# Kernel optimization log

Hardware: AMD Instinct MI355X
Metric: run time of the kernel (lower is better)

Reference implementation:

```python
import jax, jax.numpy as jnp
import numpy as np

CONV_LAYERS = 1
BI_GRU_LAYERS = 2
BN_EPS = 1e-3


def _bn(x, gamma, beta, mean, var):
    return gamma * (x - mean) * jax.lax.rsqrt(var + BN_EPS) + beta


def _gru_pass(x, Wx, Wh, b_in, b_rec, reverse=False):
    # Keras GRU: reset_after=True, recurrent_activation=sigmoid, activation=relu,
    # gate order [z, r, h]. x: [B,T,D] -> [B,T,U]
    B, T, _ = x.shape
    U = Wh.shape[0]
    if reverse:
        x = x[:, ::-1]
    xg = jnp.einsum('btd,dg->btg', x, Wx) + b_in  # [B,T,3U] input-side gates, precomputed
    xg = jnp.swapaxes(xg, 0, 1)                    # time-major [T,B,3U]

    def step(h, g):
        rg = h @ Wh + b_rec                        # recurrent-side gates [B,3U]
        xz, xr, xh = jnp.split(g, 3, axis=-1)
        rz, rr, rh = jnp.split(rg, 3, axis=-1)
        z = jax.nn.sigmoid(xz + rz)
        r = jax.nn.sigmoid(xr + rr)
        hh = jax.nn.relu(xh + r * rh)              # reset_after: r gates the recurrent term
        h = z * h + (1.0 - z) * hh
        return h, h

    h0 = jnp.zeros((B, U), x.dtype)
    _, hs = jax.lax.scan(step, h0, xg)             # [T,B,U]
    hs = jnp.swapaxes(hs, 0, 1)
    if reverse:
        hs = hs[:, ::-1]
    return hs


def setup_inputs() -> dict:
    key = jax.random.key(0)
    ks = jax.random.split(key, 16)
    B, T, F = 32, 1024, 80
    C, U, V, K = 512, 512, 1024, 11
    s = 0.02
    inp = {
        'x': jax.random.normal(ks[0], (B, T, F), jnp.float32),
        'conv_w': jax.random.normal(ks[1], (K, F, C), jnp.float32) * s,
        'conv_b': jnp.zeros((C,), jnp.float32),
        'gru_fwd_wx': jax.random.normal(ks[2], (C, 3 * U), jnp.float32) * s,
        'gru_fwd_wh': jax.random.normal(ks[3], (U, 3 * U), jnp.float32) * s,
        'gru_fwd_bi': jnp.zeros((3 * U,), jnp.float32),
        'gru_fwd_br': jnp.zeros((3 * U,), jnp.float32),
        'gru_bwd_wx': jax.random.normal(ks[4], (C, 3 * U), jnp.float32) * s,
        'gru_bwd_wh': jax.random.normal(ks[5], (U, 3 * U), jnp.float32) * s,
        'gru_bwd_bi': jnp.zeros((3 * U,), jnp.float32),
        'gru_bwd_br': jnp.zeros((3 * U,), jnp.float32),
        'gamma': jnp.ones((C,), jnp.float32) + 0.1 * jax.random.normal(ks[6], (C,), jnp.float32),
        'beta': 0.1 * jax.random.normal(ks[7], (C,), jnp.float32),
        'mov_mean': jnp.zeros((C,), jnp.float32),
        'mov_var': jnp.ones((C,), jnp.float32),
        'dense_w': jax.random.normal(ks[8], (U, V), jnp.float32) * s,
        'dense_b': jnp.zeros((V,), jnp.float32),
    }
    return inp


def reference(x, conv_w, conv_b, gru_fwd_wx, gru_fwd_wh, gru_fwd_bi, gru_fwd_br,
              gru_bwd_wx, gru_bwd_wh, gru_bwd_bi, gru_bwd_br,
              gamma, beta, mov_mean, mov_var, dense_w, dense_b):
    for _ in range(CONV_LAYERS):
        x = jax.lax.conv_general_dilated(
            x, conv_w, window_strides=(2,), padding='SAME',
            dimension_numbers=('NWC', 'WIO', 'NWC'))
        x = jax.nn.relu(x + conv_b)
    x = _bn(x, gamma, beta, mov_mean, mov_var)  # same BN layer reused in source
    for _ in range(BI_GRU_LAYERS):              # same BiGRU layer (shared weights) reused
        x = (_gru_pass(x, gru_fwd_wx, gru_fwd_wh, gru_fwd_bi, gru_fwd_br, reverse=False)
             + _gru_pass(x, gru_bwd_wx, gru_bwd_wh, gru_bwd_bi, gru_bwd_br, reverse=True))
    x = _bn(x, gamma, beta, mov_mean, mov_var)
    logits = jnp.einsum('btu,uv->btv', x, dense_w) + dense_b
    return jax.nn.softmax(logits, axis=-1)
```

## Files before the change

kernel.cpp:

```cpp
#include <hip/hip_runtime.h>
#include <hip/hip_fp16.h>

#define BB 32
#define CC 512
#define UU 512
#define GG 1536
#define VV 1024
#define TT 512
#define MM (BB*TT)
#define TIN 1024
#define FIN 80
#define EPS 1e-3f
#define SENT 0xFFFFFFFFu

typedef _Float16 h8 __attribute__((ext_vector_type(8)));
typedef float f4 __attribute__((ext_vector_type(4)));

__global__ __launch_bounds__(256) void conv_bn_k(
    const float* __restrict__ x, const float* __restrict__ w, const float* __restrict__ cb,
    const float* __restrict__ gam, const float* __restrict__ bet,
    const float* __restrict__ mu_, const float* __restrict__ var_,
    __half* __restrict__ out)
{
  __shared__ float xs[41*80];
  int tg = blockIdx.x, b = blockIdx.y, ch = blockIdx.z;
  int t0 = tg*16;
  int in0 = t0*2 - 4;
  for (int i = threadIdx.x; i < 41*80; i += 256) {
    int r = i / 80, f = i - r*80;
    int ri = in0 + r;
    xs[i] = (ri >= 0 && ri < TIN) ? x[((size_t)b*TIN + ri)*FIN + f] : 0.f;
  }
  __syncthreads();
  int c = ch*256 + threadIdx.x;
  float acc[16];
  float bv = cb[c];
#pragma unroll
  for (int i = 0; i < 16; i++) acc[i] = bv;
  for (int k = 0; k < 11; k++) {
    for (int f = 0; f < 80; f++) {
      float wv = w[((size_t)k*80 + f)*CC + c];
#pragma unroll
      for (int i = 0; i < 16; i++) acc[i] += xs[(2*i + k)*80 + f] * wv;
    }
  }
  float ga = gam[c], be = bet[c], mu = mu_[c], iv = rsqrtf(var_[c] + EPS);
#pragma unroll
  for (int i = 0; i < 16; i++) {
    float v = fmaxf(acc[i], 0.f);
    out[((size_t)b*TT + t0 + i)*CC + c] = __float2half(ga*(v - mu)*iv + be);
  }
}

__global__ __launch_bounds__(256) void prep_wx_k(
    const float* __restrict__ wxf, const float* __restrict__ wxb,
    __half* __restrict__ of, __half* __restrict__ ob)
{
  __shared__ float tile[64][65];
  int kt = blockIdx.x*64, nt = blockIdx.y*64;
  const float* src = blockIdx.z ? wxb : wxf;
  __half* dst = blockIdx.z ? ob : of;
  for (int i = threadIdx.x; i < 4096; i += 256) {
    int r = i >> 6, c = i & 63;
    tile[r][c] = src[(size_t)(kt+r)*GG + nt + c];
  }
  __syncthreads();
  for (int i = threadIdx.x; i < 4096; i += 256) {
    int r = i >> 6, c = i & 63;
    __half h = __float2half(tile[c][r]);
    dst[(size_t)(nt+r)*1024 + kt + c] = h;
    dst[(size_t)(nt+r)*1024 + 512 + kt + c] = h;
  }
}

__global__ __launch_bounds__(256) void prep_dense_k(
    const float* __restrict__ dw, const float* __restrict__ gam, const float* __restrict__ var_,
    __half* __restrict__ dst)
{
  __shared__ float tile[64][65];
  __shared__ float s64[64];
  int kt = blockIdx.x*64, nt = blockIdx.y*64;
  if (threadIdx.x < 64) {
    int k = kt + threadIdx.x;
    s64[threadIdx.x] = gam[k] * rsqrtf(var_[k] + EPS);
  }
  for (int i = threadIdx.x; i < 4096; i += 256) {
    int r = i >> 6, c = i & 63;
    tile[r][c] = dw[(size_t)(kt+r)*VV + nt + c];
  }
  __syncthreads();
  for (int i = threadIdx.x; i < 4096; i += 256) {
    int r = i >> 6, c = i & 63;
    __half h = __float2half(tile[c][r] * s64[c]);
    dst[(size_t)(nt+r)*1024 + kt + c] = h;
    dst[(size_t)(nt+r)*1024 + 512 + kt + c] = h;
  }
}

__global__ __launch_bounds__(256) void prep_bias_k(
    const float* __restrict__ dw, const float* __restrict__ db,
    const float* __restrict__ gam, const float* __restrict__ bet,
    const float* __restrict__ mu_, const float* __restrict__ var_,
    float* __restrict__ bias2)
{
  int n = blockIdx.x*256 + threadIdx.x;
  float acc = db[n];
  for (int k = 0; k < CC; k++) {
    float o = bet[k] - gam[k]*mu_[k]*rsqrtf(var_[k] + EPS);
    acc += o * dw[(size_t)k*VV + n];
  }
  bias2[n] = acc;
}

template<int OUTH>
__global__ __launch_bounds__(256,2) void hgemm_k(
    const __half* __restrict__ A, const __half* __restrict__ BT,
    const float* __restrict__ bias, void* __restrict__ Cout,
    int M, int N, int K, int lda, int ldb)
{
  __shared__ _Float16 As[2][128*40];
  __shared__ _Float16 Bs[2][128*40];
  int m0 = blockIdx.y*128, n0 = blockIdx.x*128;
  int tid = threadIdx.x;
  int l = tid & 63, w = tid >> 6;
  int wr = w >> 1, wc = w & 1;
  int srow = tid >> 1, soff = (tid & 1)*16;
  const __half* ap = A  + (size_t)(m0 + srow)*lda + soff;
  const __half* bp = BT + (size_t)(n0 + srow)*ldb + soff;
  f4 acc[4][4];
#pragma unroll
  for (int i=0;i<4;i++)
#pragma unroll
    for (int j=0;j<4;j++) acc[i][j] = (f4){0.f,0.f,0.f,0.f};

  uint4 av  = *(const uint4*)(ap);
  uint4 av2 = *(const uint4*)(ap + 8);
  uint4 bv  = *(const uint4*)(bp);
  uint4 bv2 = *(const uint4*)(bp + 8);
  *(uint4*)&As[0][srow*40 + soff]     = av;
  *(uint4*)&As[0][srow*40 + soff + 8] = av2;
  *(uint4*)&Bs[0][srow*40 + soff]     = bv;
  *(uint4*)&Bs[0][srow*40 + soff + 8] = bv2;
  __syncthreads();

  int lr = (l & 15), lk = (l >> 4)*8;
  int nk = K >> 5;
  for (int kt = 0; kt < nk; kt++) {
    int cb_ = kt & 1;
    if (kt + 1 < nk) {
      av  = *(const uint4*)(ap + kt*32 + 32);
      av2 = *(const uint4*)(ap + kt*32 + 40);
      bv  = *(const uint4*)(bp + kt*32 + 32);
      bv2 = *(const uint4*)(bp + kt*32 + 40);
    }
    h8 af[4], bf[4];
#pragma unroll
    for (int i = 0; i < 4; i++)
      af[i] = *(const h8*)&As[cb_][(wr*64 + i*16 + lr)*40 + lk];
#pragma unroll
    for (int j = 0; j < 4; j++)
      bf[j] = *(const h8*)&Bs[cb_][(wc*64 + j*16 + lr)*40 + lk];
#pragma unroll
    for (int i = 0; i < 4; i++)
#pragma unroll
      for (int j = 0; j < 4; j++)
        acc[i][j] = __builtin_amdgcn_mfma_f32_16x16x32_f16(af[i], bf[j], acc[i][j], 0, 0, 0);
    if (kt + 1 < nk) {
      *(uint4*)&As[cb_^1][srow*40 + soff]     = av;
      *(uint4*)&As[cb_^1][srow*40 + soff + 8] = av2;
      *(uint4*)&Bs[cb_^1][srow*40 + soff]     = bv;
      *(uint4*)&Bs[cb_^1][srow*40 + soff + 8] = bv2;
    }
    __syncthreads();
  }
  int cb = n0 + wc*64 + lr;
  int rb = m0 + wr*64 + (l >> 4)*4;
#pragma unroll
  for (int j = 0; j < 4; j++) {
    float bs = bias[cb + j*16];
#pragma unroll
    for (int i = 0; i < 4; i++) {
#pragma unroll
      for (int q = 0; q < 4; q++) {
        float v = acc[i][j][q] + bs;
        int row = rb + i*16 + q, col = cb + j*16;
        if (OUTH) ((__half*)Cout)[(size_t)row*N + col] = __float2half(v);
        else      ((float*)Cout)[(size_t)row*N + col] = v;
      }
    }
  }
}

__global__ __launch_bounds__(256,1) void gru_layer_k(
    const __half* __restrict__ xgf, const __half* __restrict__ xgb,
    const float* __restrict__ whf, const float* __restrict__ whb,
    const float* __restrict__ brf, const float* __restrict__ brb,
    __half* __restrict__ H,
    unsigned* __restrict__ hbL)
{
  int wg  = blockIdx.x & 7;
  int bg  = (blockIdx.x >> 3) & 3;
  int dir = blockIdx.x >> 5;
  int grp = dir*4 + bg;
  const __half* xg = dir ? xgb : xgf;
  const float* wh  = dir ? whb : whf;
  const float* brc = dir ? brb : brf;
  unsigned* hbg = hbL + (size_t)grp*8192;
  int tid = threadIdx.x;
  int L = tid & 63, wv = tid >> 6;
  int u0 = wg*64, b0 = bg*8;

  __shared__ _Float16 hsl[2][8][544];

  int urow = L & 15, kb = L >> 4;
  int ubase = u0 + wv*16;
  h8 wb[3][16];
#pragma unroll
  for (int g3 = 0; g3 < 3; g3++)
#pragma unroll
    for (int ks = 0; ks < 16; ks++) {
      h8 v;
#pragma unroll
      for (int j = 0; j < 8; j++)
        v[j] = (_Float16)wh[(size_t)(ks*32 + kb*8 + j)*GG + g3*512 + ubase + urow];
      wb[g3][ks] = v;
    }

  int b = L & 15, b7 = L & 7;
  int myu = ubase + kb*4;
  float br3[3][4];
#pragma unroll
  for (int g3 = 0; g3 < 3; g3++)
#pragma unroll
    for (int q = 0; q < 4; q++)
      br3[g3][q] = brc[g3*512 + myu + q];
  float hreg[4] = {0.f, 0.f, 0.f, 0.f};
  bool bval = b < 8;
  int upair = (u0 >> 1) + wv*8 + kb*2;

  uint2 xz2, xr2, xh2;
  {
    int t0_ = dir ? 511 : 0;
    const unsigned* xp = (const unsigned*)xg + (size_t)((b0 + b7)*TT + t0_)*768;
    xz2 = *(const uint2*)(xp + upair);
    xr2 = *(const uint2*)(xp + 256 + upair);
    xh2 = *(const uint2*)(xp + 512 + upair);
  }

  (void)__hip_atomic_exchange(&hbg[0*2048 + wg*256 + tid], 0u,
                              __ATOMIC_RELAXED, __HIP_MEMORY_SCOPE_AGENT);

  int sr = tid >> 5, sc = tid & 31;
  int sb = sc >> 2, sg0 = sr*8 + (sc & 3)*2;
  int sws0 = ((sg0 ^ sb) << 3), sws1 = (((sg0 + 1) ^ sb) << 3);

#define STAGE(PH, NB) {                                                     \
    const unsigned* gp = &hbg[(PH)*2048 + sr*256 + sc*8];                   \
    uint4 d0, d1;                                                           \
    long guard = 0;                                                         \
    for (;;) {                                                              \
      asm volatile(                                                         \
        "global_load_dwordx4 %0, %2, off sc0 sc1\n\t"                       \
        "global_load_dwordx4 %1, %2, off offset:16 sc0 sc1\n\t"             \
        "s_waitcnt vmcnt(0)"                                                \
        : "=&v"(d0), "=&v"(d1) : "v"(gp) : "memory");                       \
      bool ok = (d0.x!=SENT)&(d0.y!=SENT)&(d0.z!=SENT)&(d0.w!=SENT)         \
              & (d1.x!=SENT)&(d1.y!=SENT)&(d1.z!=SENT)&(d1.w!=SENT);        \
      if (ok || ++guard > 2000000L) break;                                  \
      if (guard > 2) __builtin_amdgcn_s_sleep(1);                           \
    }                                                                       \
    *(uint4*)&hsl[NB][sb][sws0] = d0;                                       \
    *(uint4*)&hsl[NB][sb][sws1] = d1;                                       \
  }

  STAGE(0, 0);
  __syncthreads();

  for (int s = 0; s < 512; s++) {
    int buf = s & 1;
    f4 a0 = (f4){0.f,0.f,0.f,0.f}, a1 = a0, a2 = a0;
#pragma unroll
    for (int ks = 0; ks < 16; ks++) {
      int g = ks*4 + kb;
      h8 hf = *(const h8*)&hsl[buf][b7][(g ^ b7) << 3];
      a0 = __builtin_amdgcn_mfma_f32_16x16x32_f16(wb[0][ks], hf, a0, 0, 0, 0);
      a1 = __builtin_amdgcn_mfma_f32_16x16x32_f16(wb[1][ks], hf, a1, 0, 0, 0);
      a2 = __builtin_amdgcn_mfma_f32_16x16x32_f16(wb[2][ks], hf, a2, 0, 0, 0);
    }
    int t = dir ? (511 - s) : s;
    __half2 xzl = *(__half2*)&xz2.x, xzh = *(__half2*)&xz2.y;
    __half2 xrl = *(__half2*)&xr2.x, xrh = *(__half2*)&xr2.y;
    __half2 xhl = *(__half2*)&xh2.x, xhh = *(__half2*)&xh2.y;
    float2 fz0 = __half22float2(xzl), fz1 = __half22float2(xzh);
    float2 fr0 = __half22float2(xrl), fr1 = __half22float2(xrh);
    float2 fh0 = __half22float2(xhl), fh1 = __half22float2(xhh);
    float xzf[4] = {fz0.x, fz0.y, fz1.x, fz1.y};
    float xrf[4] = {fr0.x, fr0.y, fr1.x, fr1.y};
    float xhf[4] = {fh0.x, fh0.y, fh1.x, fh1.y};
#pragma unroll
    for (int q = 0; q < 4; q++) {
      float az = (q==0? a0[0] : q==1? a0[1] : q==2? a0[2] : a0[3]);
      float ar = (q==0? a1[0] : q==1? a1[1] : q==2? a1[2] : a1[3]);
      float ah = (q==0? a2[0] : q==1? a2[1] : q==2? a2[2] : a2[3]);
      float z = 1.f/(1.f + __expf(-(xzf[q] + br3[0][q] + az)));
      float r = 1.f/(1.f + __expf(-(xrf[q] + br3[1][q] + ar)));
      float hh = fmaxf(xhf[q] + r*(br3[2][q] + ah), 0.f);
      hreg[q] = z*hreg[q] + (1.f - z)*hh;
    }
    int pn = (s + 1) & 3;
    if (bval) {
      __half2 p01 = __floats2half2_rn(hreg[0], hreg[1]);
      __half2 p23 = __floats2half2_rn(hreg[2], hreg[3]);
      unsigned pk0 = *(unsigned*)&p01, pk1 = *(unsigned*)&p23;
      unsigned long long pkl = ((unsigned long long)pk1 << 32) | pk0;
      (void)__hip_atomic_exchange(
          (unsigned long long*)&hbg[pn*2048 + wg*256 + b*32 + wv*8 + kb*2],
          pkl, __ATOMIC_RELAXED, __HIP_MEMORY_SCOPE_AGENT);
      uint2 pv; pv.x = pk0; pv.y = pk1;
      *(uint2*)((unsigned*)H + (size_t)((b0 + b)*TT + t)*512 + dir*256 + upair) = pv;
    }
    {
      int tn = (dir ? (510 - s) : (s + 1)) & 511;
      const unsigned* xp = (const unsigned*)xg + (size_t)((b0 + b7)*TT + tn)*768;
      xz2 = *(const uint2*)(xp + upair);
      xr2 = *(const uint2*)(xp + 256 + upair);
      xh2 = *(const uint2*)(xp + 512 + upair);
    }
    if (s < 511) STAGE(pn, buf ^ 1);
    if (tid < 128)
      (void)__hip_atomic_exchange(
          (unsigned long long*)&hbg[((s+3)&3)*2048 + wg*256] + tid,
          0xFFFFFFFFFFFFFFFFull, __ATOMIC_RELAXED, __HIP_MEMORY_SCOPE_AGENT);
    __syncthreads();
  }
#undef STAGE
}

__global__ __launch_bounds__(256) void softmax_k(float* __restrict__ p) {
  size_t row = blockIdx.x;
  float* pr = p + row*VV;
  int tid = threadIdx.x;
  float4 v = ((float4*)pr)[tid];
  float m = fmaxf(fmaxf(v.x, v.y), fmaxf(v.z, v.w));
#pragma unroll
  for (int o = 32; o >= 1; o >>= 1) m = fmaxf(m, __shfl_xor(m, o));
  __shared__ float red[4];
  __shared__ float red2[4];
  int w = tid >> 6;
  if ((tid & 63) == 0) red[w] = m;
  __syncthreads();
  m = fmaxf(fmaxf(red[0], red[1]), fmaxf(red[2], red[3]));
  v.x = __expf(v.x - m); v.y = __expf(v.y - m);
  v.z = __expf(v.z - m); v.w = __expf(v.w - m);
  float s = v.x + v.y + v.z + v.w;
#pragma unroll
  for (int o = 32; o >= 1; o >>= 1) s += __shfl_xor(s, o);
  if ((tid & 63) == 0) red2[w] = s;
  __syncthreads();
  s = red2[0] + red2[1] + red2[2] + red2[3];
  float inv = 1.f / s;
  v.x *= inv; v.y *= inv; v.z *= inv; v.w *= inv;
  ((float4*)pr)[tid] = v;
}

extern "C" void kernel_launch(void* const* d_in, const int* in_sizes, int n_in,
                              void* d_out, int out_size, void* d_ws, size_t ws_size,
                              hipStream_t stream) {
  const float* x      = (const float*)d_in[0];
  const float* conv_w = (const float*)d_in[1];
  const float* conv_b = (const float*)d_in[2];
  const float* wx_f   = (const float*)d_in[3];
  const float* wh_f   = (const float*)d_in[4];
  const float* bi_f   = (const float*)d_in[5];
  const float* br_f   = (const float*)d_in[6];
  const float* wx_b   = (const float*)d_in[7];
  const float* wh_b   = (const float*)d_in[8];
  const float* bi_b   = (const float*)d_in[9];
  const float* br_b   = (const float*)d_in[10];
  const float* gam    = (const float*)d_in[11];
  const float* bet    = (const float*)d_in[12];
  const float* mu_    = (const float*)d_in[13];
  const float* var_   = (const float*)d_in[14];
  const float* dw     = (const float*)d_in[15];
  const float* db     = (const float*)d_in[16];

  char* ws = (char*)d_ws;
  __half* xgf   = (__half*)(ws + 0);
  __half* xgb   = (__half*)(ws + 50331648LL);
  __half* WxfT2 = (__half*)(ws + 100663296LL);
  __half* WxbT2 = (__half*)(ws + 103809024LL);
  __half* DwT2  = (__half*)(ws + 106954752LL);
  float*  bias2 = (float*)(ws + 109051904LL);
  __half* c0    = (__half*)(ws + 109056000LL);
  __half* H     = (__half*)(ws + 109056000LL);
  unsigned* hb1 = (unsigned*)(ws + 142610432LL);
  unsigned* hb2 = (unsigned*)(ws + 142872576LL);
  if (ws_size < 143134720ULL) return;
  float* logits = (float*)d_out;

  (void)hipMemsetAsync(hb1, 0xFF, 524288, stream);

  prep_wx_k<<<dim3(8,24,2), 256, 0, stream>>>(wx_f, wx_b, WxfT2, WxbT2);
  prep_dense_k<<<dim3(8,16), 256, 0, stream>>>(dw, gam, var_, DwT2);
  prep_bias_k<<<4, 256, 0, stream>>>(dw, db, gam, bet, mu_, var_, bias2);

  conv_bn_k<<<dim3(32,32,2), 256, 0, stream>>>(x, conv_w, conv_b, gam, bet, mu_, var_, c0);

  hgemm_k<1><<<dim3(12,128), 256, 0, stream>>>(c0, WxfT2, bi_f, xgf, MM, GG, 512, 512, 1024);
  hgemm_k<1><<<dim3(12,128), 256, 0, stream>>>(c0, WxbT2, bi_b, xgb, MM, GG, 512, 512, 1024);
  gru_layer_k<<<64, 256, 0, stream>>>(xgf, xgb, wh_f, wh_b, br_f, br_b, H, hb1);
  hgemm_k<1><<<dim3(12,128), 256, 0, stream>>>(H, WxfT2, bi_f, xgf, MM, GG, 1024, 1024, 1024);
  hgemm_k<1><<<dim3(12,128), 256, 0, stream>>>(H, WxbT2, bi_b, xgb, MM, GG, 1024, 1024, 1024);
  gru_layer_k<<<64, 256, 0, stream>>>(xgf, xgb, wh_f, wh_b, br_f, br_b, H, hb2);
  hgemm_k<0><<<dim3(8,128), 256, 0, stream>>>(H, DwT2, bias2, logits, MM, VV, 1024, 1024, 1024);
  softmax_k<<<MM, 256, 0, stream>>>(logits);
}
```

Before: 2.832 ms.

## Overlap next-layer projection GEMMs with GRU recurrence via persistent worker blocks

```diff
diff --git a/kernel.cpp b/kernel.cpp
--- a/kernel.cpp
+++ b/kernel.cpp
@@ -191,68 +191,142 @@
   }
 }
 
-__global__ __launch_bounds__(256,1) void gru_layer_k(
+__device__ __forceinline__ void worker_tile(
+    const unsigned short* __restrict__ Hh, const __half* __restrict__ BT,
+    const float* __restrict__ bias, void* __restrict__ Cout,
+    int m0, int n0, int N, int OUTH,
+    _Float16* As, _Float16* Bs, int tid)
+{
+  int l = tid & 63, w = tid >> 6;
+  int wr = w >> 1, wc = w & 1;
+  int srow = tid >> 1, soff = (tid & 1)*16;
+  const __half* bp = BT + (size_t)(n0 + srow)*1024 + soff;
+  const unsigned short* apB = Hh + (size_t)(m0 + srow)*1024 + soff;
+  f4 acc[4][4];
+#pragma unroll
+  for (int i=0;i<4;i++)
+#pragma unroll
+    for (int j=0;j<4;j++) acc[i][j] = (f4){0.f,0.f,0.f,0.f};
+  int lr = (l & 15), lk = (l >> 4)*8;
+  for (int kt = 0; kt < 32; kt++) {
+    uint4 a0, a1;
+    const unsigned short* gpa = apB + kt*32;
+    asm volatile(
+      "global_load_dwordx4 %0, %2, off sc0 sc1\n\t"
+      "global_load_dwordx4 %1, %2, off offset:16 sc0 sc1\n\t"
+      "s_waitcnt vmcnt(0)"
+      : "=&v"(a0), "=&v"(a1) : "v"(gpa) : "memory");
+    uint4 b0 = *(const uint4*)(bp + kt*32);
+    uint4 b1 = *(const uint4*)(bp + kt*32 + 8);
+    __syncthreads();
+    *(uint4*)&As[srow*40 + soff]     = a0;
+    *(uint4*)&As[srow*40 + soff + 8] = a1;
+    *(uint4*)&Bs[srow*40 + soff]     = b0;
+    *(uint4*)&Bs[srow*40 + soff + 8] = b1;
+    __syncthreads();
+    h8 af[4], bf[4];
+#pragma unroll
+    for (int i = 0; i < 4; i++)
+      af[i] = *(const h8*)&As[(wr*64 + i*16 + lr)*40 + lk];
+#pragma unroll
+    for (int j = 0; j < 4; j++)
+      bf[j] = *(const h8*)&Bs[(wc*64 + j*16 + lr)*40 + lk];
+#pragma unroll
+    for (int i = 0; i < 4; i++)
+#pragma unroll
+      for (int j = 0; j < 4; j++)
+        acc[i][j] = __builtin_amdgcn_mfma_f32_16x16x32_f16(af[i], bf[j], acc[i][j], 0, 0, 0);
+  }
+  int cb = n0 + wc*64 + lr;
+  int rb = m0 + wr*64 + (l >> 4)*4;
+#pragma unroll
+  for (int j = 0; j < 4; j++) {
+    float bs = bias[cb + j*16];
+#pragma unroll
+    for (int i = 0; i < 4; i++) {
+#pragma unroll
+      for (int q = 0; q < 4; q++) {
+        float v = acc[i][j][q] + bs;
+        int row = rb + i*16 + q, col = cb + j*16;
+        if (OUTH) ((__half*)Cout)[(size_t)row*N + col] = __float2half(v);
+        else      ((float*)Cout)[(size_t)row*N + col] = v;
+      }
+    }
+  }
+}
+
+template<int L>
+__global__ __launch_bounds__(256,1) void gru_fused_k(
     const __half* __restrict__ xgf, const __half* __restrict__ xgb,
     const float* __restrict__ whf, const float* __restrict__ whb,
     const float* __restrict__ brf, const float* __restrict__ brb,
     __half* __restrict__ H,
-    unsigned* __restrict__ hbL)
-{
-  int wg  = blockIdx.x & 7;
-  int bg  = (blockIdx.x >> 3) & 3;
-  int dir = blockIdx.x >> 5;
-  int grp = dir*4 + bg;
-  const __half* xg = dir ? xgb : xgf;
-  const float* wh  = dir ? whb : whf;
-  const float* brc = dir ? brb : brf;
-  unsigned* hbg = hbL + (size_t)grp*8192;
+    unsigned* __restrict__ hbL,
+    const __half* __restrict__ BTa, const __half* __restrict__ BTb,
+    const float* __restrict__ bsa, const float* __restrict__ bsb,
+    void* __restrict__ outA, void* __restrict__ outB,
+    unsigned* __restrict__ flags, unsigned* __restrict__ queue)
+{
   int tid = threadIdx.x;
-  int L = tid & 63, wv = tid >> 6;
-  int u0 = wg*64, b0 = bg*8;
-
   __shared__ _Float16 hsl[2][8][544];
-
-  int urow = L & 15, kb = L >> 4;
-  int ubase = u0 + wv*16;
-  h8 wb[3][16];
-#pragma unroll
-  for (int g3 = 0; g3 < 3; g3++)
-#pragma unroll
-    for (int ks = 0; ks < 16; ks++) {
-      h8 v;
-#pragma unroll
-      for (int j = 0; j < 8; j++)
-        v[j] = (_Float16)wh[(size_t)(ks*32 + kb*8 + j)*GG + g3*512 + ubase + urow];
-      wb[g3][ks] = v;
-    }
-
-  int b = L & 15, b7 = L & 7;
-  int myu = ubase + kb*4;
-  float br3[3][4];
-#pragma unroll
-  for (int g3 = 0; g3 < 3; g3++)
-#pragma unroll
-    for (int q = 0; q < 4; q++)
-      br3[g3][q] = brc[g3*512 + myu + q];
-  float hreg[4] = {0.f, 0.f, 0.f, 0.f};
-  bool bval = b < 8;
-  int upair = (u0 >> 1) + wv*8 + kb*2;
-
-  uint2 xz2, xr2, xh2;
-  {
-    int t0_ = dir ? 511 : 0;
-    const unsigned* xp = (const unsigned*)xg + (size_t)((b0 + b7)*TT + t0_)*768;
-    xz2 = *(const uint2*)(xp + upair);
-    xr2 = *(const uint2*)(xp + 256 + upair);
-    xh2 = *(const uint2*)(xp + 512 + upair);
-  }
-
-  (void)__hip_atomic_exchange(&hbg[0*2048 + wg*256 + tid], 0u,
-                              __ATOMIC_RELAXED, __HIP_MEMORY_SCOPE_AGENT);
-
-  int sr = tid >> 5, sc = tid & 31;
-  int sb = sc >> 2, sg0 = sr*8 + (sc & 3)*2;
-  int sws0 = ((sg0 ^ sb) << 3), sws1 = (((sg0 + 1) ^ sb) << 3);
+  __shared__ _Float16 As[128*40];
+  __shared__ _Float16 Bs[128*40];
+  __shared__ unsigned tileS;
+
+  if (blockIdx.x < 64) {
+    int wg  = blockIdx.x & 7;
+    int bg  = (blockIdx.x >> 3) & 3;
+    int dir = blockIdx.x >> 5;
+    int grp = dir*4 + bg;
+    const __half* xg = dir ? xgb : xgf;
+    const float* wh  = dir ? whb : whf;
+    const float* brc = dir ? brb : brf;
+    unsigned* hbg = hbL + (size_t)grp*8192;
+    unsigned* myflag = flags + dir*32 + bg*8 + wg;
+    int L_ = tid & 63, wv = tid >> 6;
+    int u0 = wg*64, b0 = bg*8;
+
+    int urow = L_ & 15, kb = L_ >> 4;
+    int ubase = u0 + wv*16;
+    h8 wb[3][16];
+#pragma unroll
+    for (int g3 = 0; g3 < 3; g3++)
+#pragma unroll
+      for (int ks = 0; ks < 16; ks++) {
+        h8 v;
+#pragma unroll
+        for (int j = 0; j < 8; j++)
+          v[j] = (_Float16)wh[(size_t)(ks*32 + kb*8 + j)*GG + g3*512 + ubase + urow];
+        wb[g3][ks] = v;
+      }
+
+    int b = L_ & 15, b7 = L_ & 7;
+    int myu = ubase + kb*4;
+    float br3[3][4];
+#pragma unroll
+    for (int g3 = 0; g3 < 3; g3++)
+#pragma unroll
+      for (int q = 0; q < 4; q++)
+        br3[g3][q] = brc[g3*512 + myu + q];
+    float hreg[4] = {0.f, 0.f, 0.f, 0.f};
+    bool bval = b < 8;
+    int upair = (u0 >> 1) + wv*8 + kb*2;
+
+    uint2 xz2, xr2, xh2;
+    {
+      int t0_ = dir ? 511 : 0;
+      const unsigned* xp = (const unsigned*)xg + (size_t)((b0 + b7)*TT + t0_)*768;
+      xz2 = *(const uint2*)(xp + upair);
+      xr2 = *(const uint2*)(xp + 256 + upair);
+      xh2 = *(const uint2*)(xp + 512 + upair);
+    }
+
+    (void)__hip_atomic_exchange(&hbg[0*2048 + wg*256 + tid], 0u,
+                                __ATOMIC_RELAXED, __HIP_MEMORY_SCOPE_AGENT);
+
+    int sr = tid >> 5, sc = tid & 31;
+    int sb = sc >> 2, sg0 = sr*8 + (sc & 3)*2;
+    int sws0 = ((sg0 ^ sb) << 3), sws1 = (((sg0 + 1) ^ sb) << 3);
 
 #define STAGE(PH, NB) {                                                     \
     const unsigned* gp = &hbg[(PH)*2048 + sr*256 + sc*8];                   \
@@ -273,67 +347,126 @@
     *(uint4*)&hsl[NB][sb][sws1] = d1;                                       \
   }
 
-  STAGE(0, 0);
-  __syncthreads();
-
-  for (int s = 0; s < 512; s++) {
-    int buf = s & 1;
-    f4 a0 = (f4){0.f,0.f,0.f,0.f}, a1 = a0, a2 = a0;
-#pragma unroll
-    for (int ks = 0; ks < 16; ks++) {
-      int g = ks*4 + kb;
-      h8 hf = *(const h8*)&hsl[buf][b7][(g ^ b7) << 3];
-      a0 = __builtin_amdgcn_mfma_f32_16x16x32_f16(wb[0][ks], hf, a0, 0, 0, 0);
-      a1 = __builtin_amdgcn_mfma_f32_16x16x32_f16(wb[1][ks], hf, a1, 0, 0, 0);
-      a2 = __builtin_amdgcn_mfma_f32_16x16x32_f16(wb[2][ks], hf, a2, 0, 0, 0);
-    }
-    int t = dir ? (511 - s) : s;
-    __half2 xzl = *(__half2*)&xz2.x, xzh = *(__half2*)&xz2.y;
-    __half2 xrl = *(__half2*)&xr2.x, xrh = *(__half2*)&xr2.y;
-    __half2 xhl = *(__half2*)&xh2.x, xhh = *(__half2*)&xh2.y;
-    float2 fz0 = __half22float2(xzl), fz1 = __half22float2(xzh);
-    float2 fr0 = __half22float2(xrl), fr1 = __half22float2(xrh);
-    float2 fh0 = __half22float2(xhl), fh1 = __half22float2(xhh);
-    float xzf[4] = {fz0.x, fz0.y, fz1.x, fz1.y};
-    float xrf[4] = {fr0.x, fr0.y, fr1.x, fr1.y};
-    float xhf[4] = {fh0.x, fh0.y, fh1.x, fh1.y};
-#pragma unroll
-    for (int q = 0; q < 4; q++) {
-      float az = (q==0? a0[0] : q==1? a0[1] : q==2? a0[2] : a0[3]);
-      float ar = (q==0? a1[0] : q==1? a1[1] : q==2? a1[2] : a1[3]);
-      float ah = (q==0? a2[0] : q==1? a2[1] : q==2? a2[2] : a2[3]);
-      float z = 1.f/(1.f + __expf(-(xzf[q] + br3[0][q] + az)));
-      float r = 1.f/(1.f + __expf(-(xrf[q] + br3[1][q] + ar)));
-      float hh = fmaxf(xhf[q] + r*(br3[2][q] + ah), 0.f);
-      hreg[q] = z*hreg[q] + (1.f - z)*hh;
-    }
-    int pn = (s + 1) & 3;
-    if (bval) {
-      __half2 p01 = __floats2half2_rn(hreg[0], hreg[1]);
-      __half2 p23 = __floats2half2_rn(hreg[2], hreg[3]);
-      unsigned pk0 = *(unsigned*)&p01, pk1 = *(unsigned*)&p23;
-      unsigned long long pkl = ((unsigned long long)pk1 << 32) | pk0;
-      (void)__hip_atomic_exchange(
-          (unsigned long long*)&hbg[pn*2048 + wg*256 + b*32 + wv*8 + kb*2],
-          pkl, __ATOMIC_RELAXED, __HIP_MEMORY_SCOPE_AGENT);
-      uint2 pv; pv.x = pk0; pv.y = pk1;
-      *(uint2*)((unsigned*)H + (size_t)((b0 + b)*TT + t)*512 + dir*256 + upair) = pv;
-    }
-    {
-      int tn = (dir ? (510 - s) : (s + 1)) & 511;
-      const unsigned* xp = (const unsigned*)xg + (size_t)((b0 + b7)*TT + tn)*768;
-      xz2 = *(const uint2*)(xp + upair);
-      xr2 = *(const uint2*)(xp + 256 + upair);
-      xh2 = *(const uint2*)(xp + 512 + upair);
-    }
-    if (s < 511) STAGE(pn, buf ^ 1);
-    if (tid < 128)
-      (void)__hip_atomic_exchange(
-          (unsigned long long*)&hbg[((s+3)&3)*2048 + wg*256] + tid,
-          0xFFFFFFFFFFFFFFFFull, __ATOMIC_RELAXED, __HIP_MEMORY_SCOPE_AGENT);
-    __syncthreads();
-  }
+    STAGE(0, 0);
+    __syncthreads();
+
+    for (int s = 0; s < 512; s++) {
+      int buf = s & 1;
+      if (tid == 0)
+        __hip_atomic_store(myflag, (unsigned)s,
+                           __ATOMIC_RELAXED, __HIP_MEMORY_SCOPE_AGENT);
+      f4 a0 = (f4){0.f,0.f,0.f,0.f}, a1 = a0, a2 = a0;
+#pragma unroll
+      for (int ks = 0; ks < 16; ks++) {
+        int g = ks*4 + kb;
+        h8 hf = *(const h8*)&hsl[buf][b7][(g ^ b7) << 3];
+        a0 = __builtin_amdgcn_mfma_f32_16x16x32_f16(wb[0][ks], hf, a0, 0, 0, 0);
+        a1 = __builtin_amdgcn_mfma_f32_16x16x32_f16(wb[1][ks], hf, a1, 0, 0, 0);
+        a2 = __builtin_amdgcn_mfma_f32_16x16x32_f16(wb[2][ks], hf, a2, 0, 0, 0);
+      }
+      int t = dir ? (511 - s) : s;
+      __half2 xzl = *(__half2*)&xz2.x, xzh = *(__half2*)&xz2.y;
+      __half2 xrl = *(__half2*)&xr2.x, xrh = *(__half2*)&xr2.y;
+      __half2 xhl = *(__half2*)&xh2.x, xhh = *(__half2*)&xh2.y;
+      float2 fz0 = __half22float2(xzl), fz1 = __half22float2(xzh);
+      float2 fr0 = __half22float2(xrl), fr1 = __half22float2(xrh);
+      float2 fh0 = __half22float2(xhl), fh1 = __half22float2(xhh);
+      float xzf[4] = {fz0.x, fz0.y, fz1.x, fz1.y};
+      float xrf[4] = {fr0.x, fr0.y, fr1.x, fr1.y};
+      float xhf[4] = {fh0.x, fh0.y, fh1.x, fh1.y};
+#pragma unroll
+      for (int q = 0; q < 4; q++) {
+        float az = (q==0? a0[0] : q==1? a0[1] : q==2? a0[2] : a0[3]);
+        float ar = (q==0? a1[0] : q==1? a1[1] : q==2? a1[2] : a1[3]);
+        float ah = (q==0? a2[0] : q==1? a2[1] : q==2? a2[2] : a2[3]);
+        float z = 1.f/(1.f + __expf(-(xzf[q] + br3[0][q] + az)));
+        float r = 1.f/(1.f + __expf(-(xrf[q] + br3[1][q] + ar)));
+        float hh = fmaxf(xhf[q] + r*(br3[2][q] + ah), 0.f);
+        hreg[q] = z*hreg[q] + (1.f - z)*hh;
+      }
+      int pn = (s + 1) & 3;
+      if (bval) {
+        __half2 p01 = __floats2half2_rn(hreg[0], hreg[1]);
+        __half2 p23 = __floats2half2_rn(hreg[2], hreg[3]);
+        unsigned pk0 = *(unsigned*)&p01, pk1 = *(unsigned*)&p23;
+        unsigned long long pkl = ((unsigned long long)pk1 << 32) | pk0;
+        (void)__hip_atomic_exchange(
+            (unsigned long long*)&hbg[pn*2048 + wg*256 + b*32 + wv*8 + kb*2],
+            pkl, __ATOMIC_RELAXED, __HIP_MEMORY_SCOPE_AGENT);
+        __hip_atomic_store(
+            (unsigned long long*)((unsigned*)H + (size_t)((b0 + b)*TT + t)*512
+                                  + dir*256 + upair),
+            pkl, __ATOMIC_RELAXED, __HIP_MEMORY_SCOPE_AGENT);
+      }
+      {
+        int tn = (dir ? (510 - s) : (s + 1)) & 511;
+        const unsigned* xp = (const unsigned*)xg + (size_t)((b0 + b7)*TT + tn)*768;
+        xz2 = *(const uint2*)(xp + upair);
+        xr2 = *(const uint2*)(xp + 256 + upair);
+        xh2 = *(const uint2*)(xp + 512 + upair);
+      }
+      if (s < 511) STAGE(pn, buf ^ 1);
+      if (tid < 128)
+        (void)__hip_atomic_exchange(
+            (unsigned long long*)&hbg[((s+3)&3)*2048 + wg*256] + tid,
+            0xFFFFFFFFFFFFFFFFull, __ATOMIC_RELAXED, __HIP_MEMORY_SCOPE_AGENT);
+      __syncthreads();
+    }
 #undef STAGE
+    if (tid == 0)
+      __hip_atomic_store(myflag, 512u, __ATOMIC_RELAXED, __HIP_MEMORY_SCOPE_AGENT);
+  }
+
+  const int NT = (L == 1) ? 3072 : 1024;
+  for (;;) {
+    __syncthreads();
+    if (tid == 0)
+      tileS = __hip_atomic_fetch_add(queue, 1u, __ATOMIC_RELAXED,
+                                     __HIP_MEMORY_SCOPE_AGENT);
+    __syncthreads();
+    unsigned tv = tileS;
+    if (tv >= (unsigned)NT) break;
+    int b, tb, nt, g;
+    if (L == 1) {
+      int half = tv >= 1536; int i = half ? (int)tv - 1536 : (int)tv;
+      g = i & 1; i >>= 1; nt = i % 12; int bm = i / 12;
+      b = bm >> 1; tb = half ? ((bm & 1) ? 3 : 0) : (1 + (bm & 1));
+    } else {
+      int half = tv >= 512; int i = half ? (int)tv - 512 : (int)tv;
+      g = 0; nt = i & 7; int bm = i >> 3;
+      b = bm >> 1; tb = half ? ((bm & 1) ? 3 : 0) : (1 + (bm & 1));
+    }
+    int tlo = tb*128, thi = tlo + 128;
+    int bgx = b >> 3;
+    if (tid == 0) {
+      const unsigned* ff = flags + bgx*8;
+      const unsigned* fb = flags + 32 + bgx*8;
+      long guard = 0;
+      for (;;) {
+        unsigned mf = 0xFFFFFFFFu, mb = 0xFFFFFFFFu;
+#pragma unroll
+        for (int i2 = 0; i2 < 8; i2++) {
+          unsigned a = __hip_atomic_load(ff + i2, __ATOMIC_RELAXED,
+                                         __HIP_MEMORY_SCOPE_AGENT);
+          unsigned c = __hip_atomic_load(fb + i2, __ATOMIC_RELAXED,
+                                         __HIP_MEMORY_SCOPE_AGENT);
+          mf = a < mf ? a : mf; mb = c < mb ? c : mb;
+        }
+        if (mf >= (unsigned)thi && mb >= (unsigned)(512 - tlo)) break;
+        if (++guard > 30000000L) break;
+        __builtin_amdgcn_s_sleep(16);
+      }
+    }
+    __syncthreads();
+    int m0 = (b*4 + tb) * 128;
+    int n0 = nt * 128;
+    if (L == 1)
+      worker_tile((const unsigned short*)H, g ? BTb : BTa, g ? bsb : bsa,
+                  g ? outB : outA, m0, n0, GG, 1, As, Bs, tid);
+    else
+      worker_tile((const unsigned short*)H, BTa, bsa, outA, m0, n0, VV, 0,
+                  As, Bs, tid);
+  }
 }
 
 __global__ __launch_bounds__(256) void softmax_k(float* __restrict__ p) {
@@ -395,10 +528,15 @@
   __half* H     = (__half*)(ws + 109056000LL);
   unsigned* hb1 = (unsigned*)(ws + 142610432LL);
   unsigned* hb2 = (unsigned*)(ws + 142872576LL);
-  if (ws_size < 143134720ULL) return;
+  unsigned* fl1 = (unsigned*)(ws + 143134720LL);
+  unsigned* fl2 = (unsigned*)(ws + 143134976LL);
+  unsigned* q1  = (unsigned*)(ws + 143135232LL);
+  unsigned* q2  = (unsigned*)(ws + 143135296LL);
+  if (ws_size < 143135360ULL) return;
   float* logits = (float*)d_out;
 
   (void)hipMemsetAsync(hb1, 0xFF, 524288, stream);
+  (void)hipMemsetAsync(fl1, 0, 640, stream);
 
   prep_wx_k<<<dim3(8,24,2), 256, 0, stream>>>(wx_f, wx_b, WxfT2, WxbT2);
   prep_dense_k<<<dim3(8,16), 256, 0, stream>>>(dw, gam, var_, DwT2);
@@ -408,10 +546,11 @@
 
   hgemm_k<1><<<dim3(12,128), 256, 0, stream>>>(c0, WxfT2, bi_f, xgf, MM, GG, 512, 512, 1024);
   hgemm_k<1><<<dim3(12,128), 256, 0, stream>>>(c0, WxbT2, bi_b, xgb, MM, GG, 512, 512, 1024);
-  gru_layer_k<<<64, 256, 0, stream>>>(xgf, xgb, wh_f, wh_b, br_f, br_b, H, hb1);
-  hgemm_k<1><<<dim3(12,128), 256, 0, stream>>>(H, WxfT2, bi_f, xgf, MM, GG, 1024, 1024, 1024);
-  hgemm_k<1><<<dim3(12,128), 256, 0, stream>>>(H, WxbT2, bi_b, xgb, MM, GG, 1024, 1024, 1024);
-  gru_layer_k<<<64, 256, 0, stream>>>(xgf, xgb, wh_f, wh_b, br_f, br_b, H, hb2);
-  hgemm_k<0><<<dim3(8,128), 256, 0, stream>>>(H, DwT2, bias2, logits, MM, VV, 1024, 1024, 1024);
+  gru_fused_k<1><<<256, 256, 0, stream>>>(xgf, xgb, wh_f, wh_b, br_f, br_b,
+                                          H, hb1, WxfT2, WxbT2, bi_f, bi_b,
+                                          xgf, xgb, fl1, q1);
+  gru_fused_k<2><<<256, 256, 0, stream>>>(xgf, xgb, wh_f, wh_b, br_f, br_b,
+                                          H, hb2, DwT2, nullptr, bias2, nullptr,
+                                          logits, nullptr, fl2, q2);
   softmax_k<<<MM, 256, 0, stream>>>(logits);
 }
```

After: 5.822 ms. 106% more time.
